# Kernel tuning notes

Hardware: AMD Instinct MI355X
Metric: run time of the kernel (lower is better)

Reference implementation:

```python
import jax, jax.numpy as jnp
import numpy as np


def log_g(x):
    # log of g(x) = where(x>=0, x+0.5, sigmoid(x))
    return jnp.where(x >= 0, jnp.log(jax.nn.relu(x) + 0.5), -jax.nn.softplus(-x))


def heinsen_scan_log(log_coeffs, log_values):
    # associative scan in log space over seq dim (axis=1)
    a_star = jnp.cumsum(log_coeffs, axis=1)
    log_h0_plus_b_star = jax.lax.cumlogsumexp(log_values - a_star, axis=1)
    return jnp.exp(a_star + log_h0_plus_b_star)


def setup_inputs() -> dict:
    key = jax.random.key(0)
    k1, k2, k3 = jax.random.split(key, 3)
    B, S, D_IN, D_INNER, D_OUT = 4, 4096, 1024, 1024, 1024
    x = jax.random.normal(k1, (B, S, D_IN), dtype=jnp.float32)
    # xavier_normal for Linear(d_in, 2*d_inner): std = sqrt(2/(fan_in+fan_out))
    std_hg = float(np.sqrt(2.0 / (D_IN + 2 * D_INNER)))
    W_hg = jax.random.normal(k2, (2 * D_INNER, D_IN), dtype=jnp.float32) * std_hg
    std_out = float(np.sqrt(2.0 / (D_INNER + D_OUT)))
    W_out = jax.random.normal(k3, (D_OUT, D_INNER), dtype=jnp.float32) * std_out
    return {"x": x, "W_hg": W_hg, "W_out": W_out}


def reference(x, W_hg, W_out):
    # x: [B,S,Din]; W_hg: [2*Dinner, Din]; W_out: [Dout, Dinner]
    hg = jnp.einsum("bsd,ed->bse", x, W_hg)
    hidden, gate = jnp.split(hg, 2, axis=-1)
    log_coeffs = -jax.nn.softplus(gate)        # log(1 - z)
    log_z = -jax.nn.softplus(-gate)            # log(z)
    log_values = log_z + log_g(hidden)
    h = heinsen_scan_log(log_coeffs, log_values)  # [B,S,Dinner]
    out = jnp.einsum("bsd,od->bso", h, W_out)
    return out
```

## Files before the change

### kernel.cpp

```cpp
#include <hip/hip_runtime.h>
#include <math.h>


typedef unsigned short ushort_t;
typedef __attribute__((ext_vector_type(4))) float f32x4;
typedef __attribute__((ext_vector_type(8))) __bf16 bf16x8;
typedef __attribute__((ext_vector_type(8))) unsigned short u16x8;

constexpr int Bsz  = 4;
constexpr int S    = 4096;
constexpr int Din  = 1024;
constexpr int Dh   = 1024;
constexpr int M    = Bsz * S;
constexpr int NCH  = 64;
constexpr int CL   = S / NCH;

__device__ __forceinline__ unsigned short f2bf(float f) {
    unsigned int u = __float_as_uint(f);
    unsigned int r = (u + 0x7fffu + ((u >> 16) & 1u)) >> 16;
    return (unsigned short)r;
}
__device__ __forceinline__ float bf2f(unsigned short u) {
    return __uint_as_float(((unsigned int)u) << 16);
}
__device__ __forceinline__ float sigf(float x) {
    x = fminf(fmaxf(x, -30.f), 30.f);
    return 1.0f / (1.0f + __expf(-x));
}
__device__ __forceinline__ void gld_lds16(const ushort_t* g, ushort_t* l) {
    __builtin_amdgcn_global_load_lds(
        (const __attribute__((address_space(1))) void*)g,
        (__attribute__((address_space(3))) void*)l, 16, 0, 0);
}

__global__ __launch_bounds__(256) void cvt_all(
    const float* __restrict__ x, const float* __restrict__ whg,
    const float* __restrict__ wout,
    ushort_t* __restrict__ xb, ushort_t* __restrict__ whgb,
    ushort_t* __restrict__ woutb)
{
    constexpr int NX = M * Din / 8;
    constexpr int NW = 2048 * 1024 / 8;
    const int i = blockIdx.x * 256 + threadIdx.x;
    const float* src; ushort_t* dst; int k;
    if (i < NX)            { src = x;    dst = xb;    k = i; }
    else if (i < NX + NW)  { src = whg;  dst = whgb;  k = i - NX; }
    else                   { src = wout; dst = woutb; k = i - NX - NW; }
    const float4 a = ((const float4*)src)[(size_t)k * 2];
    const float4 b = ((const float4*)src)[(size_t)k * 2 + 1];
    u16x8 o;
    o[0] = f2bf(a.x); o[1] = f2bf(a.y); o[2] = f2bf(a.z); o[3] = f2bf(a.w);
    o[4] = f2bf(b.x); o[5] = f2bf(b.y); o[6] = f2bf(b.z); o[7] = f2bf(b.w);
    ((u16x8*)dst)[k] = o;
}

__global__ __launch_bounds__(512, 2) void gemm256(
    const ushort_t* __restrict__ A, int lda,
    const ushort_t* __restrict__ B, int ldb,
    ushort_t* __restrict__ Cout, int ldc, int K, int nbx_log2)
{
    __shared__ ushort_t lds[4][2][8192];

    const int P = K >> 5;

    const int nwg = gridDim.x;
    const int cpx = nwg >> 3;
    const int bid = blockIdx.x;
    const int swz = (bid & 7) * cpx + (bid >> 3);
    const int bx  = swz & ((1 << nbx_log2) - 1);
    const int by  = swz >> nbx_log2;
    const int bm0 = by * 256;
    const int bn0 = bx * 256;

    const int t  = threadIdx.x;
    const int w  = t >> 6;
    const int l  = t & 63;
    const int wr = w >> 1;
    const int wr3 = w >> 2;
    const int wc = w & 3;
    (void)wr;

    const int fr = l & 15;
    const int kg = l >> 4;
    const int qp = kg ^ (((fr >> 3) & 1) << 1);
    const int a_base = wr3 * 4096 + fr * 32 + qp * 8;
    const int b_base = wc * 2048 + fr * 32 + qp * 8;

    const int rs = l >> 2;
    const int lq = (l & 3) ^ (((rs >> 3) & 1) << 1);
    const ushort_t* gA0 = A + (size_t)(bm0 + w * 16 + rs) * lda + lq * 8;
    const ushort_t* gA1 = gA0 + (size_t)128 * lda;
    const ushort_t* gB0 = B + (size_t)(bn0 + w * 16 + rs) * ldb + lq * 8;
    const ushort_t* gB1 = gB0 + (size_t)128 * ldb;

    f32x4 acc[8][4];
    #pragma unroll
    for (int i = 0; i < 8; ++i)
        #pragma unroll
        for (int j = 0; j < 4; ++j)
            acc[i][j] = (f32x4){0.f, 0.f, 0.f, 0.f};

    auto stage = [&](int p) {
        const int s2 = p & 3;
        const int ko = p * 32;
        gld_lds16(gA0 + ko, &lds[s2][0][w * 512]);
        gld_lds16(gA1 + ko, &lds[s2][0][w * 512 + 4096]);
        gld_lds16(gB0 + ko, &lds[s2][1][w * 512]);
        gld_lds16(gB1 + ko, &lds[s2][1][w * 512 + 4096]);
    };

    auto phase_body = [&](int p, bool do_stage) {
        __builtin_amdgcn_s_barrier();
        __builtin_amdgcn_sched_barrier(0);
        const int s = p & 3;
        const ushort_t* la = &lds[s][0][0];
        const ushort_t* lb = &lds[s][1][0];
        bf16x8 af[8], bfr[4];
        #pragma unroll
        for (int i = 0; i < 8; ++i)
            af[i] = *reinterpret_cast<const bf16x8*>(&la[a_base + i * 512]);
        #pragma unroll
        for (int j = 0; j < 4; ++j)
            bfr[j] = *reinterpret_cast<const bf16x8*>(&lb[b_base + j * 512]);
        if (do_stage) stage(p + 2);
        __builtin_amdgcn_sched_barrier(0);
        __builtin_amdgcn_s_setprio(1);
        #pragma unroll
        for (int i = 0; i < 8; ++i)
            #pragma unroll
            for (int j = 0; j < 4; ++j)
                acc[i][j] = __builtin_amdgcn_mfma_f32_16x16x32_bf16(
                    af[i], bfr[j], acc[i][j], 0, 0, 0);
        __builtin_amdgcn_s_setprio(0);
        __builtin_amdgcn_sched_barrier(0);
    };

    stage(0);
    stage(1);

    for (int p = 0; p < P - 1; ++p) {
        asm volatile("s_waitcnt vmcnt(4)" ::: "memory");
        phase_body(p, p < P - 2);
    }
    asm volatile("s_waitcnt vmcnt(0)" ::: "memory");
    phase_body(P - 1, false);

    #pragma unroll
    for (int i = 0; i < 8; ++i) {
        #pragma unroll
        for (int j = 0; j < 4; ++j) {
            const int col = bn0 + wc * 64 + j * 16 + fr;
            #pragma unroll
            for (int r = 0; r < 4; ++r) {
                const int row = bm0 + wr3 * 128 + i * 16 + kg * 4 + r;
                Cout[(size_t)row * ldc + col] = f2bf(acc[i][j][r]);
            }
        }
    }
}

__global__ __launch_bounds__(512, 4) void gemm128(
    const ushort_t* __restrict__ A, int lda,
    const ushort_t* __restrict__ B, int ldb,
    float* __restrict__ Cout, int ldc, int K, int nbx_log2)
{
    constexpr int AEL = 128 * 32;
    __shared__ ushort_t lds[2][AEL + 8192];

    const int P = K >> 5;

    const int nwg = gridDim.x;
    const int cpx = nwg >> 3;
    const int bid = blockIdx.x;
    const int swz = (bid & 7) * cpx + (bid >> 3);
    const int bx  = swz & ((1 << nbx_log2) - 1);
    const int by  = swz >> nbx_log2;
    const int bm0 = by * 128;
    const int bn0 = bx * 256;

    const int t  = threadIdx.x;
    const int w  = t >> 6;
    const int l  = t & 63;
    const int wr = w >> 2;
    const int wc = w & 3;

    const int fr = l & 15;
    const int kg = l >> 4;
    const int qp = kg ^ (((fr >> 3) & 1) << 1);
    const int a_base = wr * 2048 + fr * 32 + qp * 8;
    const int b_base = wc * 2048 + fr * 32 + qp * 8;

    const int rs = l >> 2;
    const int lq = (l & 3) ^ (((rs >> 3) & 1) << 1);
    const ushort_t* gA0 = A + (size_t)(bm0 + w * 16 + rs) * lda + lq * 8;
    const ushort_t* gB0 = B + (size_t)(bn0 + w * 16 + rs) * ldb + lq * 8;
    const ushort_t* gB1 = gB0 + (size_t)128 * ldb;

    f32x4 acc[4][4];
    #pragma unroll
    for (int i = 0; i < 4; ++i)
        #pragma unroll
        for (int j = 0; j < 4; ++j)
            acc[i][j] = (f32x4){0.f, 0.f, 0.f, 0.f};

    auto stage = [&](int p) {
        ushort_t* base = &lds[p & 1][0];
        const int ko = p * 32;
        gld_lds16(gA0 + ko, base + w * 512);
        gld_lds16(gB0 + ko, base + AEL + w * 512);
        gld_lds16(gB1 + ko, base + AEL + w * 512 + 4096);
    };

    stage(0);
    asm volatile("s_waitcnt vmcnt(0)" ::: "memory");
    __builtin_amdgcn_s_barrier();

    #pragma unroll 1
    for (int p = 0; p < P; ++p) {
        const ushort_t* la = &lds[p & 1][0];
        const ushort_t* lb = la + AEL;
        __builtin_amdgcn_sched_barrier(0);
        bf16x8 af[4], bfr[4];
        #pragma unroll
        for (int i = 0; i < 4; ++i)
            af[i] = *reinterpret_cast<const bf16x8*>(&la[a_base + i * 512]);
        #pragma unroll
        for (int j = 0; j < 4; ++j)
            bfr[j] = *reinterpret_cast<const bf16x8*>(&lb[b_base + j * 512]);
        if (p + 1 < P) stage(p + 1);
        __builtin_amdgcn_sched_barrier(0);
        __builtin_amdgcn_s_setprio(1);
        #pragma unroll
        for (int i = 0; i < 4; ++i)
            #pragma unroll
            for (int j = 0; j < 4; ++j)
                acc[i][j] = __builtin_amdgcn_mfma_f32_16x16x32_bf16(
                    af[i], bfr[j], acc[i][j], 0, 0, 0);
        __builtin_amdgcn_s_setprio(0);
        __builtin_amdgcn_sched_barrier(0);
        if (p + 1 < P) {
            asm volatile("s_waitcnt vmcnt(0)" ::: "memory");
            __builtin_amdgcn_s_barrier();
        }
    }

    #pragma unroll
    for (int i = 0; i < 4; ++i) {
        #pragma unroll
        for (int j = 0; j < 4; ++j) {
            const int col = bn0 + wc * 64 + j * 16 + fr;
            #pragma unroll
            for (int r = 0; r < 4; ++r) {
                const int row = bm0 + wr * 64 + i * 16 + kg * 4 + r;
                Cout[(size_t)row * ldc + col] = acc[i][j][r];
            }
        }
    }
}


__global__ __launch_bounds__(256) void scan_stage1(
    const ushort_t* __restrict__ hg, float* __restrict__ Abuf,
    float* __restrict__ hlbuf)
{
    const int g     = blockIdx.x * 256 + threadIdx.x;
    const int d     = g & (Dh - 1);
    const int chunk = (g >> 10) & (NCH - 1);
    const int b     = g >> 16;
    const size_t rowbase = (size_t)(b * S + chunk * CL) * 2048;
    float h = 0.0f, Aacc = 1.0f;
    #pragma unroll 4
    for (int i = 0; i < CL; ++i) {
        const float hid  = bf2f(hg[rowbase + (size_t)i * 2048 + d]);
        const float gate = bf2f(hg[rowbase + (size_t)i * 2048 + 1024 + d]);
        const float z  = sigf(gate);
        const float c  = sigf(-gate);
        const float gv = (hid >= 0.0f) ? (hid + 0.5f) : sigf(hid);
        h = fmaf(c, h, z * gv);
        Aacc *= c;
    }
    const size_t o = (size_t)(b * NCH + chunk) * Dh + d;
    Abuf[o]  = Aacc;
    hlbuf[o] = h;
}

__global__ __launch_bounds__(256) void scan_stage2(
    const float* __restrict__ Abuf, const float* __restrict__ hlbuf,
    float* __restrict__ Hs)
{
    const int g = blockIdx.x * 256 + threadIdx.x;
    const int d = g & (Dh - 1);
    const int b = g >> 10;
    float h = 0.0f;
    for (int ch = 0; ch < NCH; ++ch) {
        const size_t o = (size_t)(b * NCH + ch) * Dh + d;
        Hs[o] = h;
        h = fmaf(Abuf[o], h, hlbuf[o]);
    }
}

__global__ __launch_bounds__(256) void scan_stage3(
    const ushort_t* __restrict__ hg, const float* __restrict__ Hs,
    ushort_t* __restrict__ hout)
{
    const int g     = blockIdx.x * 256 + threadIdx.x;
    const int d     = g & (Dh - 1);
    const int chunk = (g >> 10) & (NCH - 1);
    const int b     = g >> 16;
    const size_t rowbase = (size_t)(b * S + chunk * CL) * 2048;
    const size_t hbase   = (size_t)(b * S + chunk * CL) * 1024 + d;
    float h = Hs[(size_t)(b * NCH + chunk) * Dh + d];
    #pragma unroll 4
    for (int i = 0; i < CL; ++i) {
        const size_t ro = rowbase + (size_t)i * 2048;
        const float hid  = bf2f(hg[ro + d]);
        const float gate = bf2f(hg[ro + 1024 + d]);
        const float z  = sigf(gate);
        const float c  = sigf(-gate);
        const float gv = (hid >= 0.0f) ? (hid + 0.5f) : sigf(hid);
        h = fmaf(c, h, z * gv);
        hout[hbase + (size_t)i * 1024] = f2bf(h);
    }
}

extern "C" void kernel_launch(void* const* d_in, const int* in_sizes, int n_in,
                              void* d_out, int out_size, void* d_ws, size_t ws_size,
                              hipStream_t stream)
{
    (void)in_sizes; (void)n_in; (void)out_size; (void)ws_size;
    const float* x    = (const float*)d_in[0];
    const float* Whg  = (const float*)d_in[1];
    const float* Wout = (const float*)d_in[2];
    float* out = (float*)d_out;

    ushort_t* hgbuf = (ushort_t*)d_ws;
    ushort_t* xb    = hgbuf + (size_t)M * 2048;
    ushort_t* whgb  = xb + (size_t)M * 1024;
    ushort_t* woutb = whgb + (size_t)2048 * 1024;
    float*    Abuf  = (float*)(woutb + (size_t)1024 * 1024);
    float*    hlbuf = Abuf + (size_t)Bsz * NCH * Dh;
    float*    Hsbuf = hlbuf + (size_t)Bsz * NCH * Dh;

    const dim3 blk(256);

    cvt_all<<<dim3(9728), blk, 0, stream>>>(x, Whg, Wout, xb, whgb, woutb);

    gemm256<<<dim3(512), dim3(512), 0, stream>>>(
        xb, Din, whgb, Din, hgbuf, 2048, Din, 3);

    scan_stage1<<<dim3(Bsz * NCH * Dh / 256), blk, 0, stream>>>(hgbuf, Abuf, hlbuf);
    scan_stage2<<<dim3(Bsz * Dh / 256), blk, 0, stream>>>(Abuf, hlbuf, Hsbuf);
    scan_stage3<<<dim3(Bsz * NCH * Dh / 256), blk, 0, stream>>>(hgbuf, Hsbuf, xb);

    gemm128<<<dim3(512), dim3(512), 0, stream>>>(
        xb, Dh, woutb, Din, out, 1024, Dh, 2);
}
```

Baseline: 214.6 us.

## Fuse three-stage chunked scan into one kernel with flag-based decoupled lookback

Replaces the three scan kernels with a single kernel. Each block computes its chunk's carry, publishes it through agent-scope atomics and a flag, then spins until all earlier chunks are published and recombines their carries before the final pass. Each thread now handles two channels with 32-bit packed bf16 loads and stores. Separately, gemm128 moves from double to triple LDS buffering, prefetching two stages ahead with one barrier per iteration. The spin-wait relies on all 512 blocks being co-resident, which is a deadlock risk if they are not, and the flags need a memset every call.

```diff
diff --git a/kernel.cpp b/kernel.cpp
--- a/kernel.cpp
+++ b/kernel.cpp
@@ -3,6 +3,7 @@
 
 
 typedef unsigned short ushort_t;
+typedef unsigned int uint_t;
 typedef __attribute__((ext_vector_type(4))) float f32x4;
 typedef __attribute__((ext_vector_type(8))) __bf16 bf16x8;
 typedef __attribute__((ext_vector_type(8))) unsigned short u16x8;
@@ -75,15 +76,13 @@
     const int t  = threadIdx.x;
     const int w  = t >> 6;
     const int l  = t & 63;
-    const int wr = w >> 1;
-    const int wr3 = w >> 2;
+    const int wr = w >> 2;
     const int wc = w & 3;
-    (void)wr;
 
     const int fr = l & 15;
     const int kg = l >> 4;
     const int qp = kg ^ (((fr >> 3) & 1) << 1);
-    const int a_base = wr3 * 4096 + fr * 32 + qp * 8;
+    const int a_base = wr * 4096 + fr * 32 + qp * 8;
     const int b_base = wc * 2048 + fr * 32 + qp * 8;
 
     const int rs = l >> 2;
@@ -152,7 +151,7 @@
             const int col = bn0 + wc * 64 + j * 16 + fr;
             #pragma unroll
             for (int r = 0; r < 4; ++r) {
-                const int row = bm0 + wr3 * 128 + i * 16 + kg * 4 + r;
+                const int row = bm0 + wr * 128 + i * 16 + kg * 4 + r;
                 Cout[(size_t)row * ldc + col] = f2bf(acc[i][j][r]);
             }
         }
@@ -164,8 +163,7 @@
     const ushort_t* __restrict__ B, int ldb,
     float* __restrict__ Cout, int ldc, int K, int nbx_log2)
 {
-    constexpr int AEL = 128 * 32;
-    __shared__ ushort_t lds[2][AEL + 8192];
+    __shared__ ushort_t lds[3][12288];
 
     const int P = K >> 5;
 
@@ -188,7 +186,7 @@
     const int kg = l >> 4;
     const int qp = kg ^ (((fr >> 3) & 1) << 1);
     const int a_base = wr * 2048 + fr * 32 + qp * 8;
-    const int b_base = wc * 2048 + fr * 32 + qp * 8;
+    const int b_base = 4096 + wc * 2048 + fr * 32 + qp * 8;
 
     const int rs = l >> 2;
     const int lq = (l & 3) ^ (((rs >> 3) & 1) << 1);
@@ -203,31 +201,36 @@
         for (int j = 0; j < 4; ++j)
             acc[i][j] = (f32x4){0.f, 0.f, 0.f, 0.f};
 
-    auto stage = [&](int p) {
-        ushort_t* base = &lds[p & 1][0];
+    auto stage = [&](int p, int s) {
+        ushort_t* base = &lds[s][0];
         const int ko = p * 32;
         gld_lds16(gA0 + ko, base + w * 512);
-        gld_lds16(gB0 + ko, base + AEL + w * 512);
-        gld_lds16(gB1 + ko, base + AEL + w * 512 + 4096);
+        gld_lds16(gB0 + ko, base + 4096 + w * 512);
+        gld_lds16(gB1 + ko, base + 8192 + w * 512);
     };
 
-    stage(0);
-    asm volatile("s_waitcnt vmcnt(0)" ::: "memory");
-    __builtin_amdgcn_s_barrier();
-
+    stage(0, 0);
+    stage(1, 1);
+
+    int scur = 0;
+    int snxt2 = 2;
     #pragma unroll 1
     for (int p = 0; p < P; ++p) {
-        const ushort_t* la = &lds[p & 1][0];
-        const ushort_t* lb = la + AEL;
-        __builtin_amdgcn_sched_barrier(0);
+        if (p < P - 1)
+            asm volatile("s_waitcnt vmcnt(3)" ::: "memory");
+        else
+            asm volatile("s_waitcnt vmcnt(0)" ::: "memory");
+        __builtin_amdgcn_s_barrier();
+        __builtin_amdgcn_sched_barrier(0);
+        const ushort_t* ls = &lds[scur][0];
         bf16x8 af[4], bfr[4];
         #pragma unroll
         for (int i = 0; i < 4; ++i)
-            af[i] = *reinterpret_cast<const bf16x8*>(&la[a_base + i * 512]);
+            af[i] = *reinterpret_cast<const bf16x8*>(&ls[a_base + i * 512]);
         #pragma unroll
         for (int j = 0; j < 4; ++j)
-            bfr[j] = *reinterpret_cast<const bf16x8*>(&lb[b_base + j * 512]);
-        if (p + 1 < P) stage(p + 1);
+            bfr[j] = *reinterpret_cast<const bf16x8*>(&ls[b_base + j * 512]);
+        if (p + 2 < P) stage(p + 2, snxt2);
         __builtin_amdgcn_sched_barrier(0);
         __builtin_amdgcn_s_setprio(1);
         #pragma unroll
@@ -238,10 +241,8 @@
                     af[i], bfr[j], acc[i][j], 0, 0, 0);
         __builtin_amdgcn_s_setprio(0);
         __builtin_amdgcn_sched_barrier(0);
-        if (p + 1 < P) {
-            asm volatile("s_waitcnt vmcnt(0)" ::: "memory");
-            __builtin_amdgcn_s_barrier();
-        }
+        scur  = (scur  == 2) ? 0 : scur + 1;
+        snxt2 = (snxt2 == 2) ? 0 : snxt2 + 1;
     }
 
     #pragma unroll
@@ -258,68 +259,84 @@
     }
 }
 
-
-__global__ __launch_bounds__(256) void scan_stage1(
-    const ushort_t* __restrict__ hg, float* __restrict__ Abuf,
-    float* __restrict__ hlbuf)
-{
-    const int g     = blockIdx.x * 256 + threadIdx.x;
-    const int d     = g & (Dh - 1);
-    const int chunk = (g >> 10) & (NCH - 1);
-    const int b     = g >> 16;
-    const size_t rowbase = (size_t)(b * S + chunk * CL) * 2048;
-    float h = 0.0f, Aacc = 1.0f;
+__global__ __launch_bounds__(256) void scan_fused(
+    const ushort_t* __restrict__ hg, float* __restrict__ Apart,
+    float* __restrict__ hlpart, int* __restrict__ flags,
+    ushort_t* __restrict__ hout)
+{
+    const int bid   = blockIdx.x;
+    const int half  = bid & 1;
+    const int chunk = (bid >> 1) & (NCH - 1);
+    const int b     = bid >> 7;
+    const int t     = threadIdx.x;
+    const int d     = half * 512 + 2 * t;
+    const size_t rowbase = (size_t)(b * S + chunk * CL) * 2048 + d;
+
+    float h0 = 0.f, h1 = 0.f, A0 = 1.f, A1 = 1.f;
     #pragma unroll 4
     for (int i = 0; i < CL; ++i) {
-        const float hid  = bf2f(hg[rowbase + (size_t)i * 2048 + d]);
-        const float gate = bf2f(hg[rowbase + (size_t)i * 2048 + 1024 + d]);
-        const float z  = sigf(gate);
-        const float c  = sigf(-gate);
-        const float gv = (hid >= 0.0f) ? (hid + 0.5f) : sigf(hid);
-        h = fmaf(c, h, z * gv);
-        Aacc *= c;
-    }
-    const size_t o = (size_t)(b * NCH + chunk) * Dh + d;
-    Abuf[o]  = Aacc;
-    hlbuf[o] = h;
-}
-
-__global__ __launch_bounds__(256) void scan_stage2(
-    const float* __restrict__ Abuf, const float* __restrict__ hlbuf,
-    float* __restrict__ Hs)
-{
-    const int g = blockIdx.x * 256 + threadIdx.x;
-    const int d = g & (Dh - 1);
-    const int b = g >> 10;
-    float h = 0.0f;
-    for (int ch = 0; ch < NCH; ++ch) {
-        const size_t o = (size_t)(b * NCH + ch) * Dh + d;
-        Hs[o] = h;
-        h = fmaf(Abuf[o], h, hlbuf[o]);
-    }
-}
-
-__global__ __launch_bounds__(256) void scan_stage3(
-    const ushort_t* __restrict__ hg, const float* __restrict__ Hs,
-    ushort_t* __restrict__ hout)
-{
-    const int g     = blockIdx.x * 256 + threadIdx.x;
-    const int d     = g & (Dh - 1);
-    const int chunk = (g >> 10) & (NCH - 1);
-    const int b     = g >> 16;
-    const size_t rowbase = (size_t)(b * S + chunk * CL) * 2048;
-    const size_t hbase   = (size_t)(b * S + chunk * CL) * 1024 + d;
-    float h = Hs[(size_t)(b * NCH + chunk) * Dh + d];
+        const ushort_t* rp = hg + rowbase + (size_t)i * 2048;
+        const uint_t hp = *(const uint_t*)rp;
+        const uint_t gp = *(const uint_t*)(rp + 1024);
+        const float hid0 = bf2f((ushort_t)hp), hid1 = bf2f((ushort_t)(hp >> 16));
+        const float g0 = bf2f((ushort_t)gp),  g1 = bf2f((ushort_t)(gp >> 16));
+        const float c0 = sigf(-g0), z0 = 1.f - c0;
+        const float c1 = sigf(-g1), z1 = 1.f - c1;
+        const float gv0 = (hid0 >= 0.f) ? (hid0 + 0.5f) : sigf(hid0);
+        const float gv1 = (hid1 >= 0.f) ? (hid1 + 0.5f) : sigf(hid1);
+        h0 = fmaf(c0, h0, z0 * gv0);  A0 *= c0;
+        h1 = fmaf(c1, h1, z1 * gv1);  A1 *= c1;
+    }
+
+    const size_t pb = (size_t)(b * NCH + chunk) * 1024 + d;
+    __hip_atomic_store(&Apart[pb],      A0, __ATOMIC_RELAXED, __HIP_MEMORY_SCOPE_AGENT);
+    __hip_atomic_store(&Apart[pb + 1],  A1, __ATOMIC_RELAXED, __HIP_MEMORY_SCOPE_AGENT);
+    __hip_atomic_store(&hlpart[pb],     h0, __ATOMIC_RELAXED, __HIP_MEMORY_SCOPE_AGENT);
+    __hip_atomic_store(&hlpart[pb + 1], h1, __ATOMIC_RELAXED, __HIP_MEMORY_SCOPE_AGENT);
+    __syncthreads();
+    const int frow = (b * 2 + half) * NCH;
+    if (t == 0) {
+        __threadfence();
+        __hip_atomic_store(&flags[frow + chunk], 1,
+                           __ATOMIC_RELEASE, __HIP_MEMORY_SCOPE_AGENT);
+    }
+
+    while (!__syncthreads_and(
+        (t >= chunk) ||
+        __hip_atomic_load(&flags[frow + t], __ATOMIC_ACQUIRE,
+                          __HIP_MEMORY_SCOPE_AGENT) != 0)) {
+        __builtin_amdgcn_s_sleep(2);
+    }
+
+    float p0 = 0.f, p1 = 0.f;
+    #pragma unroll 4
+    for (int j = 0; j < chunk; ++j) {
+        const size_t jb = (size_t)(b * NCH + j) * 1024 + d;
+        const float Aj0 = __hip_atomic_load(&Apart[jb],      __ATOMIC_RELAXED, __HIP_MEMORY_SCOPE_AGENT);
+        const float Aj1 = __hip_atomic_load(&Apart[jb + 1],  __ATOMIC_RELAXED, __HIP_MEMORY_SCOPE_AGENT);
+        const float hj0 = __hip_atomic_load(&hlpart[jb],     __ATOMIC_RELAXED, __HIP_MEMORY_SCOPE_AGENT);
+        const float hj1 = __hip_atomic_load(&hlpart[jb + 1], __ATOMIC_RELAXED, __HIP_MEMORY_SCOPE_AGENT);
+        p0 = fmaf(Aj0, p0, hj0);
+        p1 = fmaf(Aj1, p1, hj1);
+    }
+
+    const size_t hb = (size_t)(b * S + chunk * CL) * 1024 + d;
+    h0 = p0; h1 = p1;
     #pragma unroll 4
     for (int i = 0; i < CL; ++i) {
-        const size_t ro = rowbase + (size_t)i * 2048;
-        const float hid  = bf2f(hg[ro + d]);
-        const float gate = bf2f(hg[ro + 1024 + d]);
-        const float z  = sigf(gate);
-        const float c  = sigf(-gate);
-        const float gv = (hid >= 0.0f) ? (hid + 0.5f) : sigf(hid);
-        h = fmaf(c, h, z * gv);
-        hout[hbase + (size_t)i * 1024] = f2bf(h);
+        const ushort_t* rp = hg + rowbase + (size_t)i * 2048;
+        const uint_t hp = *(const uint_t*)rp;
+        const uint_t gp = *(const uint_t*)(rp + 1024);
+        const float hid0 = bf2f((ushort_t)hp), hid1 = bf2f((ushort_t)(hp >> 16));
+        const float g0 = bf2f((ushort_t)gp),  g1 = bf2f((ushort_t)(gp >> 16));
+        const float c0 = sigf(-g0), z0 = 1.f - c0;
+        const float c1 = sigf(-g1), z1 = 1.f - c1;
+        const float gv0 = (hid0 >= 0.f) ? (hid0 + 0.5f) : sigf(hid0);
+        const float gv1 = (hid1 >= 0.f) ? (hid1 + 0.5f) : sigf(hid1);
+        h0 = fmaf(c0, h0, z0 * gv0);
+        h1 = fmaf(c1, h1, z1 * gv1);
+        const uint_t o = (uint_t)f2bf(h0) | ((uint_t)f2bf(h1) << 16);
+        *(uint_t*)(hout + hb + (size_t)i * 1024) = o;
     }
 }
 
@@ -337,20 +354,20 @@
     ushort_t* xb    = hgbuf + (size_t)M * 2048;
     ushort_t* whgb  = xb + (size_t)M * 1024;
     ushort_t* woutb = whgb + (size_t)2048 * 1024;
-    float*    Abuf  = (float*)(woutb + (size_t)1024 * 1024);
-    float*    hlbuf = Abuf + (size_t)Bsz * NCH * Dh;
-    float*    Hsbuf = hlbuf + (size_t)Bsz * NCH * Dh;
+    float*    Apart = (float*)(woutb + (size_t)1024 * 1024);
+    float*    hlprt = Apart + (size_t)Bsz * NCH * Dh;
+    int*      flags = (int*)(hlprt + (size_t)Bsz * NCH * Dh);
 
     const dim3 blk(256);
+
+    hipMemsetAsync(flags, 0, Bsz * 2 * NCH * sizeof(int), stream);
 
     cvt_all<<<dim3(9728), blk, 0, stream>>>(x, Whg, Wout, xb, whgb, woutb);
 
     gemm256<<<dim3(512), dim3(512), 0, stream>>>(
         xb, Din, whgb, Din, hgbuf, 2048, Din, 3);
 
-    scan_stage1<<<dim3(Bsz * NCH * Dh / 256), blk, 0, stream>>>(hgbuf, Abuf, hlbuf);
-    scan_stage2<<<dim3(Bsz * Dh / 256), blk, 0, stream>>>(Abuf, hlbuf, Hsbuf);
-    scan_stage3<<<dim3(Bsz * NCH * Dh / 256), blk, 0, stream>>>(hgbuf, Hsbuf, xb);
+    scan_fused<<<dim3(512), blk, 0, stream>>>(hgbuf, Apart, hlprt, flags, xb);
 
     gemm128<<<dim3(512), dim3(512), 0, stream>>>(
         xb, Dh, woutb, Din, out, 1024, Dh, 2);
```

New measurement: 245.3 us. +14.3%, slower.
